# Performance work log

Hardware: AMD Instinct MI355X
Metric: run time of the kernel (lower is better)

The kernel has to match this reference:

```python
import jax, jax.numpy as jnp
import numpy as np

WINDOW_SIZES = [4, 8, 12]
BN_EPS = 1e-5


def conv1x1(x, w, b):
    # x: [B,C,H,W], w: [O,C], b: [O]
    return jnp.einsum('bchw,oc->bohw', x, w) + b[None, :, None, None]


def bnorm(x, gamma, beta, mean, var):
    inv = gamma * jax.lax.rsqrt(var + BN_EPS)
    return (x - mean[None, :, None, None]) * inv[None, :, None, None] + beta[None, :, None, None]


def shift5(x):
    # ShiftConv2d1 depthwise fixed-weight conv == 4-direction zero-padded shift + identity
    b, c, H, W = x.shape
    g = c // 5
    p = jnp.pad(x, ((0, 0), (0, 0), (1, 1), (1, 1)))
    return jnp.concatenate([
        p[:, 0 * g:1 * g, 1:-1, 2:],    # kernel[1,2]: x[i, j+1]
        p[:, 1 * g:2 * g, 1:-1, :-2],   # kernel[1,0]: x[i, j-1]
        p[:, 2 * g:3 * g, 2:, 1:-1],    # kernel[2,1]: x[i+1, j]
        p[:, 3 * g:4 * g, :-2, 1:-1],   # kernel[0,1]: x[i-1, j]
        p[:, 4 * g:, 1:-1, 1:-1],       # kernel[1,1]: identity
    ], axis=1)


def lfe(x, w0, b0, w1, b1):
    y = jax.nn.relu(conv1x1(shift5(x), w0, b0))
    return conv1x1(shift5(y), w1, b1)


def win_part(x, ws):
    # [B,C,H,W] -> [B*nh*nw, ws*ws, C]
    b, c, H, W = x.shape
    x = x.reshape(b, c, H // ws, ws, W // ws, ws)
    return x.transpose(0, 2, 4, 3, 5, 1).reshape(b * (H // ws) * (W // ws), ws * ws, c)


def win_merge(y, ws, b, H, W):
    # [B*nh*nw, ws*ws, C] -> [B,C,H,W]
    c = y.shape[-1]
    y = y.reshape(b, H // ws, W // ws, ws, ws, c)
    return y.transpose(0, 5, 1, 3, 2, 4).reshape(b, c, H, W)


def gmsa_first(x, pi_w, pi_b, bn_g, bn_b, bn_m, bn_v, po_w, po_b):
    b, c, H, W = x.shape
    xp = bnorm(conv1x1(x, pi_w, pi_b), bn_g, bn_b, bn_m, bn_v)
    ch = 2 * c // 3
    ys, atns = [], []
    for i, ws in enumerate(WINDOW_SIZES):
        x_ = xp[:, i * ch:(i + 1) * ch]
        x_ = jnp.roll(x_, (-(ws // 2), -(ws // 2)), axis=(2, 3))
        qv = win_part(x_, ws)                      # [nw, ws*ws, 2*cc]
        cc = ch // 2
        q, v = qv[..., :cc], qv[..., cc:]
        atn = jax.nn.softmax(q @ q.transpose(0, 2, 1), axis=-1)
        y_ = win_merge(atn @ v, ws, b, H, W)
        y_ = jnp.roll(y_, (ws // 2, ws // 2), axis=(2, 3))
        ys.append(y_)
        atns.append(atn)
    return conv1x1(jnp.concatenate(ys, axis=1), po_w, po_b), atns


def gmsa_shared(x, atns, pi_w, pi_b, bn_g, bn_b, bn_m, bn_v, po_w, po_b):
    b, c, H, W = x.shape
    xp = bnorm(conv1x1(x, pi_w, pi_b), bn_g, bn_b, bn_m, bn_v)
    ch = c // 3
    ys = []
    for i, ws in enumerate(WINDOW_SIZES):
        x_ = jnp.roll(xp[:, i * ch:(i + 1) * ch], (-(ws // 2), -(ws // 2)), axis=(2, 3))
        v = win_part(x_, ws)
        y_ = win_merge(atns[i] @ v, ws, b, H, W)
        ys.append(jnp.roll(y_, (ws // 2, ws // 2), axis=(2, 3)))
    return conv1x1(jnp.concatenate(ys, axis=1), po_w, po_b)


def setup_inputs() -> dict:
    key = jax.random.key(0)
    ks = jax.random.split(key, 20)
    B, C, H, W = 4, 60, 384, 384
    E = 2 * C  # exp_ratio=2 hidden width
    s = 0.05

    def rn(k, shape):
        return jax.random.normal(k, shape, dtype=jnp.float32) * s

    return {
        'x': jax.random.normal(ks[0], (B, C, H, W), dtype=jnp.float32),
        # LFE 0
        'lfe0_w0': rn(ks[1], (E, C)), 'lfe0_b0': jnp.zeros((E,), jnp.float32),
        'lfe0_w1': rn(ks[2], (C, E)), 'lfe0_b1': jnp.zeros((C,), jnp.float32),
        # GMSA 0 (calc_attn=True): project_inp C->2C, BN(2C), project_out C->C
        'g0_pi_w': rn(ks[3], (2 * C, C)), 'g0_pi_b': jnp.zeros((2 * C,), jnp.float32),
        'g0_bn_g': jnp.ones((2 * C,), jnp.float32), 'g0_bn_b': jnp.zeros((2 * C,), jnp.float32),
        'g0_bn_m': jnp.zeros((2 * C,), jnp.float32), 'g0_bn_v': jnp.ones((2 * C,), jnp.float32),
        'g0_po_w': rn(ks[4], (C, C)), 'g0_po_b': jnp.zeros((C,), jnp.float32),
        # LFE 1
        'lfe1_w0': rn(ks[5], (E, C)), 'lfe1_b0': jnp.zeros((E,), jnp.float32),
        'lfe1_w1': rn(ks[6], (C, E)), 'lfe1_b1': jnp.zeros((C,), jnp.float32),
        # GMSA 1 (calc_attn=False): project_inp C->C, BN(C), project_out C->C
        'g1_pi_w': rn(ks[7], (C, C)), 'g1_pi_b': jnp.zeros((C,), jnp.float32),
        'g1_bn_g': jnp.ones((C,), jnp.float32), 'g1_bn_b': jnp.zeros((C,), jnp.float32),
        'g1_bn_m': jnp.zeros((C,), jnp.float32), 'g1_bn_v': jnp.ones((C,), jnp.float32),
        'g1_po_w': rn(ks[8], (C, C)), 'g1_po_b': jnp.zeros((C,), jnp.float32),
    }


def reference(x, lfe0_w0, lfe0_b0, lfe0_w1, lfe0_b1,
              g0_pi_w, g0_pi_b, g0_bn_g, g0_bn_b, g0_bn_m, g0_bn_v, g0_po_w, g0_po_b,
              lfe1_w0, lfe1_b0, lfe1_w1, lfe1_b1,
              g1_pi_w, g1_pi_b, g1_bn_g, g1_bn_b, g1_bn_m, g1_bn_v, g1_po_w, g1_po_b):
    # depth 0
    x = lfe(x, lfe0_w0, lfe0_b0, lfe0_w1, lfe0_b1) + x
    y, atns = gmsa_first(x, g0_pi_w, g0_pi_b, g0_bn_g, g0_bn_b, g0_bn_m, g0_bn_v, g0_po_w, g0_po_b)
    x = y + x
    # shared depth 1 (reuses attention maps)
    x = lfe(x, lfe1_w0, lfe1_b0, lfe1_w1, lfe1_b1) + x
    y = gmsa_shared(x, atns, g1_pi_w, g1_pi_b, g1_bn_g, g1_bn_b, g1_bn_m, g1_bn_v, g1_po_w, g1_po_b)
    return y + x
```

## Files before the change

### kernel.cpp

```cpp
#include <hip/hip_runtime.h>
#include <math.h>

constexpr int B_ = 4, C_ = 60, H_ = 384, W_ = 384;
constexpr int HW_ = H_ * W_;
constexpr int NC_ = B_ * C_ * HW_;
constexpr int NE_ = B_ * 120 * HW_;

typedef __attribute__((ext_vector_type(8))) short short8;
typedef __attribute__((ext_vector_type(4))) float f32x4;
typedef __attribute__((ext_vector_type(4))) unsigned short u16x4;

__device__ __forceinline__ unsigned short f2b(float f) {
    unsigned u = __builtin_bit_cast(unsigned, f);
    unsigned r = (u + 0x7fff + ((u >> 16) & 1)) >> 16;
    return (unsigned short)r;
}
__device__ __forceinline__ float b2f(unsigned short s) {
    return __builtin_bit_cast(float, (unsigned)s << 16);
}

__device__ __forceinline__ int xcd_swz(int bid, int nwg) {
    const int q = nwg >> 3, r = nwg & 7;
    const int xcd = bid & 7, off = bid >> 3;
    return (xcd < r ? xcd * (q + 1) : r * (q + 1) + (xcd - r) * q) + off;
}

struct PrepJobs {
    const float* src[8];
    unsigned short* dst[8];
    int cin[8];
    int cout[8];
};

__global__ __launch_bounds__(256) void prep_all(PrepJobs J)
{
    int bid = blockIdx.x;
    #pragma unroll 1
    for (int j = 0; j < 8; ++j) {
        const int KP = J.cin[j]  > 64 ? 128 : 64;
        const int MP = J.cout[j] > 64 ? 128 : 64;
        const int nb = MP * KP / 256;
        if (bid < nb) {
            const int i = bid * 256 + threadIdx.x;
            const int o = i / KP, c = i - o * KP;
            const float v = (o < J.cout[j] && c < J.cin[j]) ? J.src[j][o * J.cin[j] + c] : 0.f;
            J.dst[j][o * KP + (c ^ ((o & 7) << 3))] = f2b(v);
            return;
        }
        bid -= nb;
    }
}

struct ABJobs {
    const float* bias[8];
    const float* g[8];
    const float* bb[8];
    const float* m[8];
    const float* v[8];
    float* dst[8];
    int cout[8];
};

__global__ __launch_bounds__(256) void prep_ab(ABJobs J)
{
    const int j = blockIdx.x;
    const int n = J.cout[j];
    for (int o = threadIdx.x; o < n; o += 256) {
        float A = 1.f, Bv = J.bias[j][o];
        if (J.g[j]) {
            const float s = J.g[j][o] * rsqrtf(J.v[j][o] + 1e-5f);
            A  = s;
            Bv = (Bv - J.m[j][o]) * s + J.bb[j][o];
        }
        J.dst[j][o]     = A;
        J.dst[j][n + o] = Bv;
    }
}

template<int KP>
__device__ __forceinline__ int lds_off(int px, int cb) {
    return px * (KP * 2) + (cb ^ ((px & 7) << 4) ^ (((px >> 3) & 1) << 6));
}

template<int CIN, int COUT, int GSH, bool SRCB, bool RELU, bool RESID,
         bool RESIDB, bool OUTB>
__global__ __launch_bounds__(512, 6)
void conv_g(const void* __restrict__ in_, const unsigned short* __restrict__ wp,
            const float* __restrict__ AB,
            const void* __restrict__ resid_, void* __restrict__ out_)
{
    constexpr int KP  = CIN  > 64 ? 128 : 64;
    constexpr int MP  = COUT > 64 ? 128 : 64;
    constexpr int NNT = MP / 16;
    constexpr int KBL = KP / 32;
    __shared__ __align__(16) char xlds[128 * KP * 2];

    const int tid = threadIdx.x;
    const int n0  = blockIdx.x * 128;
    const int b   = n0 / HW_;
    const int p0  = n0 - b * HW_;
    const int hh  = p0 / W_;
    const int ww0 = p0 - hh * W_;

    for (int task = tid; task < (KP / 2) * 16; task += 512) {
        const int oct = (task >> 4) & 15;
        const int pr  = (task & 15) | ((task >> 8) << 4);
        const int c0  = pr * 2;
        const int s0  = oct * 8;

        if (c0 >= CIN) {
            #pragma unroll
            for (int i = 0; i < 8; ++i)
                *(unsigned*)(xlds + lds_off<KP>(s0 + i, c0 * 2)) = 0u;
            continue;
        }

        int dh = 0, dw = 0;
        if (GSH > 0) {
            const int grp = c0 / GSH;
            dh = (grp == 2) ? 1 : ((grp == 3) ? -1 : 0);
            dw = (grp == 0) ? 1 : ((grp == 1) ? -1 : 0);
        }
        const int h2 = hh + dh;
        const bool vh = (unsigned)h2 < (unsigned)H_;
        const long eoff = (long)(b * CIN + c0) * HW_ + h2 * W_ + ww0 + s0;

        unsigned short va[8], vb[8];
        if (vh) {
            if constexpr (SRCB) {
                const unsigned short* p = (const unsigned short*)in_;
                short8 A = *(const short8*)(p + eoff);
                short8 Bv = *(const short8*)(p + eoff + HW_);
                #pragma unroll
                for (int i = 0; i < 8; ++i) { va[i] = (unsigned short)A[i]; vb[i] = (unsigned short)Bv[i]; }
            } else {
                const float* p = (const float*)in_;
                f32x4 A0 = *(const f32x4*)(p + eoff);
                f32x4 A1 = *(const f32x4*)(p + eoff + 4);
                f32x4 B0 = *(const f32x4*)(p + eoff + HW_);
                f32x4 B1 = *(const f32x4*)(p + eoff + HW_ + 4);
                #pragma unroll
                for (int i = 0; i < 4; ++i) {
                    va[i] = f2b(A0[i]); va[i + 4] = f2b(A1[i]);
                    vb[i] = f2b(B0[i]); vb[i + 4] = f2b(B1[i]);
                }
            }
        } else {
            #pragma unroll
            for (int i = 0; i < 8; ++i) { va[i] = 0; vb[i] = 0; }
        }
        #pragma unroll
        for (int i = 0; i < 8; ++i) {
            const int px = s0 + i - dw;
            if ((unsigned)px < 128u) {
                const unsigned v = (unsigned)va[i] | ((unsigned)vb[i] << 16);
                *(unsigned*)(xlds + lds_off<KP>(px, c0 * 2)) = v;
            }
        }
        if (GSH > 0 && dw != 0) {
            const bool hndl = (dw == 1) ? (oct == 15) : (oct == 0);
            if (hndl) {
                const int px_e = (dw == 1) ? 127 : 0;
                const int w_abs = ww0 + px_e + dw;
                unsigned short ua = 0, ub = 0;
                if (vh && (unsigned)w_abs < (unsigned)W_) {
                    const long e2 = (long)(b * CIN + c0) * HW_ + h2 * W_ + w_abs;
                    if constexpr (SRCB) {
                        ua = ((const unsigned short*)in_)[e2];
                        ub = ((const unsigned short*)in_)[e2 + HW_];
                    } else {
                        ua = f2b(((const float*)in_)[e2]);
                        ub = f2b(((const float*)in_)[e2 + HW_]);
                    }
                }
                *(unsigned*)(xlds + lds_off<KP>(px_e, c0 * 2)) =
                    (unsigned)ua | ((unsigned)ub << 16);
            }
        }
    }
    __syncthreads();

    const int wv = tid >> 6, lo = tid & 15, hi = (tid & 63) >> 4;
    f32x4 acc[NNT];
    #pragma unroll
    for (int nt = 0; nt < NNT; ++nt) acc[nt] = f32x4{0.f, 0.f, 0.f, 0.f};

    #pragma unroll
    for (int kb = 0; kb < KBL; ++kb) {
        const int row = wv * 16 + lo;
        const short8 a = *(const short8*)(xlds + lds_off<KP>(row, kb * 64 + hi * 16));
        #pragma unroll
        for (int nt = 0; nt < NNT; ++nt) {
            const int wrow = nt * 16 + lo;
            const short8 bb = *(const short8*)((const char*)wp +
                      wrow * (KP * 2) + ((kb * 64 + hi * 16) ^ ((wrow & 7) << 4)));
            acc[nt] = __builtin_amdgcn_mfma_f32_16x16x32_bf16(a, bb, acc[nt], 0, 0, 0);
        }
    }

    const int px0 = p0 + wv * 16 + hi * 4;
    #pragma unroll
    for (int nt = 0; nt < NNT; ++nt) {
        const int ch = nt * 16 + lo;
        if (ch < COUT) {
            const long oi = (long)(b * COUT + ch) * HW_ + px0;
            float v[4];
            f32x4 rf;
            u16x4 rb;
            if (RESID) {
                if (RESIDB) rb = *(const u16x4*)((const unsigned short*)resid_ + oi);
                else        rf = *(const f32x4*)((const float*)resid_ + oi);
            }
            #pragma unroll
            for (int r = 0; r < 4; ++r) {
                float t = fmaf(acc[nt][r], AB[ch], AB[COUT + ch]);
                if (RELU) t = fmaxf(t, 0.f);
                if (RESID) t += RESIDB ? b2f(rb[r]) : rf[r];
                v[r] = t;
            }
            if (OUTB) {
                u16x4 o4;
                #pragma unroll
                for (int r = 0; r < 4; ++r) o4[r] = f2b(v[r]);
                *(u16x4*)((unsigned short*)out_ + oi) = o4;
            } else {
                *(f32x4*)((float*)out_ + oi) = f32x4{v[0], v[1], v[2], v[3]};
            }
        }
    }
}

template<int WS, int WPB>
__global__ __launch_bounds__(256)
void attn_m(const unsigned short* __restrict__ qsrc, int qC, int qbase,
            const unsigned short* __restrict__ vsrc, int vC, int vbase,
            unsigned short* __restrict__ out, int obase)
{
    constexpr int P     = WS * WS;
    constexpr int NMT   = P / 16;
    constexpr int S     = WS / 2;
    constexpr int WGX   = W_ / WS;
    constexpr int WGY   = H_ / WS;
    constexpr int NWIN  = WGY * WGX;
    constexpr int QP    = 40;
    constexpr int KP2   = ((P + 31) / 32) * 32;
    constexpr int VP    = KP2 + 8;
    constexpr int KB2   = KP2 / 32;
    constexpr int TILES = WPB * NMT;

    __shared__ __align__(16) unsigned short Qs[WPB * P * QP];
    __shared__ __align__(16) unsigned short VTs[WPB * 32 * VP];
    __shared__ __align__(16) unsigned short Ps[WPB * P * VP];
    __shared__ float rs[WPB * P];

    const int tid = threadIdx.x;
    const int blk = xcd_swz(blockIdx.x, gridDim.x);

    for (int i = tid; i < WPB * P * 6; i += 256) {
        const int row = i / 6, j = i - (i / 6) * 6;
        *(unsigned*)&Qs[row * QP + 20 + 2 * j] = 0u;
    }
    for (int i = tid; i < WPB * 12 * (KP2 / 2); i += 256) {
        const int rr = i / (KP2 / 2), j = i - rr * (KP2 / 2);
        const int win = rr / 12, ch = 20 + (rr - (rr / 12) * 12);
        *(unsigned*)&VTs[(win * 32 + ch) * VP + 2 * j] = 0u;
    }
    if constexpr (KP2 > P) {
        for (int i = tid; i < WPB * 20 * ((KP2 - P) / 2); i += 256) {
            const int rr = i / ((KP2 - P) / 2), j = i - rr * ((KP2 - P) / 2);
            const int win = rr / 20, ch = rr - (rr / 20) * 20;
            *(unsigned*)&VTs[(win * 32 + ch) * VP + P + 2 * j] = 0u;
        }
        for (int i = tid; i < WPB * P * ((KP2 - P) / 2); i += 256) {
            const int row = i / ((KP2 - P) / 2), j = i - row * ((KP2 - P) / 2);
            *(unsigned*)&Ps[row * VP + P + 2 * j] = 0u;
        }
    }
    for (int e = tid; e < WPB * P * 20; e += 256) {
        const int win = e / (P * 20);
        const int rem = e - win * (P * 20);
        const int ch  = rem / P;
        const int pos = rem - ch * P;
        const int gw  = blk * WPB + win;
        const int b   = gw / NWIN;
        const int rwin = gw - b * NWIN;
        const int wh = rwin / WGX, ww = rwin - (rwin / WGX) * WGX;
        const int pr = pos / WS,  pc = pos - (pos / WS) * WS;
        int hs = wh * WS + pr + S; if (hs >= H_) hs -= H_;
        int wd = ww * WS + pc + S; if (wd >= W_) wd -= W_;
        const long off = (long)hs * W_ + wd;
        Qs [(win * P  + pos) * QP + ch ] = qsrc[(long)(b * qC + qbase + ch) * HW_ + off];
        VTs[(win * 32 + ch ) * VP + pos] = vsrc[(long)(b * vC + vbase + ch) * HW_ + off];
    }
    __syncthreads();

    const int wv = tid >> 6, lo = tid & 15, hi = (tid & 63) >> 4;

    for (int t = wv; t < TILES; t += 4) {
        const int win = t / NMT, mt = t - (t / NMT) * NMT;
        const unsigned short* Qw = Qs + win * P * QP;
        unsigned short* Pw = Ps + win * P * VP;

        const short8 af = *(const short8*)(Qw + (mt * 16 + lo) * QP + hi * 8);
        f32x4 a1[NMT];
        #pragma unroll
        for (int nt = 0; nt < NMT; ++nt) a1[nt] = f32x4{0.f, 0.f, 0.f, 0.f};
        #pragma unroll
        for (int nt = 0; nt < NMT; ++nt) {
            const short8 bf = *(const short8*)(Qw + (nt * 16 + lo) * QP + hi * 8);
            a1[nt] = __builtin_amdgcn_mfma_f32_16x16x32_bf16(af, bf, a1[nt], 0, 0, 0);
        }
        float psum[4] = {0.f, 0.f, 0.f, 0.f};
        #pragma unroll
        for (int nt = 0; nt < NMT; ++nt) {
            #pragma unroll
            for (int r = 0; r < 4; ++r) {
                const float p = __expf(a1[nt][r]);
                psum[r] += p;
                Pw[(mt * 16 + hi * 4 + r) * VP + nt * 16 + lo] = f2b(p);
            }
        }
        #pragma unroll
        for (int r = 0; r < 4; ++r) {
            psum[r] += __shfl_xor(psum[r], 1);
            psum[r] += __shfl_xor(psum[r], 2);
            psum[r] += __shfl_xor(psum[r], 4);
            psum[r] += __shfl_xor(psum[r], 8);
        }
        if (lo == 0) {
            #pragma unroll
            for (int r = 0; r < 4; ++r)
                rs[win * P + mt * 16 + hi * 4 + r] = psum[r];
        }
    }
    __syncthreads();

    for (int t = wv; t < TILES; t += 4) {
        const int win = t / NMT, qt = t - (t / NMT) * NMT;
        const unsigned short* Vw = VTs + win * 32 * VP;
        const unsigned short* Pw = Ps + win * P * VP;

        f32x4 a2[2];
        a2[0] = f32x4{0.f, 0.f, 0.f, 0.f};
        a2[1] = f32x4{0.f, 0.f, 0.f, 0.f};
        #pragma unroll
        for (int kb = 0; kb < KB2; ++kb) {
            const short8 bf = *(const short8*)(Pw + (qt * 16 + lo) * VP + kb * 32 + hi * 8);
            #pragma unroll
            for (int m2 = 0; m2 < 2; ++m2) {
                const short8 af = *(const short8*)(Vw + (m2 * 16 + lo) * VP + kb * 32 + hi * 8);
                a2[m2] = __builtin_amdgcn_mfma_f32_16x16x32_bf16(af, bf, a2[m2], 0, 0, 0);
            }
        }
        const int gw = blk * WPB + win;
        const int b  = gw / NWIN;
        const int rwin = gw - b * NWIN;
        const int wh = rwin / WGX, ww = rwin - (rwin / WGX) * WGX;

        const int row = qt * 16 + lo;
        const float inv = 1.f / rs[win * P + row];
        const int pr = row / WS, pc = row - (row / WS) * WS;
        int hs = wh * WS + pr + S; if (hs >= H_) hs -= H_;
        int wd = ww * WS + pc + S; if (wd >= W_) wd -= W_;
        const long pbase = (long)(b * 60 + obase) * HW_ + (long)hs * W_ + wd;
        #pragma unroll
        for (int m2 = 0; m2 < 2; ++m2) {
            #pragma unroll
            for (int r = 0; r < 4; ++r) {
                const int ch = m2 * 16 + hi * 4 + r;
                if (ch < 20)
                    out[pbase + (long)ch * HW_] = f2b(a2[m2][r] * inv);
            }
        }
    }
}

extern "C" void kernel_launch(void* const* d_in, const int* in_sizes, int n_in,
                              void* d_out, int out_size, void* d_ws, size_t ws_size,
                              hipStream_t stream)
{
    const float* x     = (const float*)d_in[0];
    const float* l0w0  = (const float*)d_in[1];
    const float* l0b0  = (const float*)d_in[2];
    const float* l0w1  = (const float*)d_in[3];
    const float* l0b1  = (const float*)d_in[4];
    const float* g0piw = (const float*)d_in[5];
    const float* g0pib = (const float*)d_in[6];
    const float* g0bng = (const float*)d_in[7];
    const float* g0bnb = (const float*)d_in[8];
    const float* g0bnm = (const float*)d_in[9];
    const float* g0bnv = (const float*)d_in[10];
    const float* g0pow = (const float*)d_in[11];
    const float* g0pob = (const float*)d_in[12];
    const float* l1w0  = (const float*)d_in[13];
    const float* l1b0  = (const float*)d_in[14];
    const float* l1w1  = (const float*)d_in[15];
    const float* l1b1  = (const float*)d_in[16];
    const float* g1piw = (const float*)d_in[17];
    const float* g1pib = (const float*)d_in[18];
    const float* g1bng = (const float*)d_in[19];
    const float* g1bnb = (const float*)d_in[20];
    const float* g1bnm = (const float*)d_in[21];
    const float* g1bnv = (const float*)d_in[22];
    const float* g1pow = (const float*)d_in[23];
    const float* g1pob = (const float*)d_in[24];

    unsigned short* HID = (unsigned short*)d_ws;
    unsigned short* XPB = HID + NE_;
    unsigned short* XP1 = XPB + NE_;
    unsigned short* YS1 = XP1 + NC_;
    unsigned short* CCB = YS1 + NC_;
    unsigned short* WP  = CCB + NC_;
    float*          ABF = (float*)(WP + 53248);
    float* OUTF  = (float*)d_out;
    unsigned short* YS0 = (unsigned short*)d_out;

    unsigned short* W1  = WP;
    unsigned short* W2  = WP + 8192;
    unsigned short* W3  = WP + 16384;
    unsigned short* W5  = WP + 24576;
    unsigned short* W6  = WP + 28672;
    unsigned short* W7  = WP + 36864;
    unsigned short* W8  = WP + 45056;
    unsigned short* W10 = WP + 49152;

    float* AB1  = ABF;
    float* AB2  = ABF + 240;
    float* AB3  = ABF + 360;
    float* AB5  = ABF + 600;
    float* AB6  = ABF + 720;
    float* AB7  = ABF + 960;
    float* AB8  = ABF + 1080;
    float* AB10 = ABF + 1200;

    PrepJobs J;
    J.src[0]=l0w0;  J.dst[0]=W1;  J.cin[0]=60;  J.cout[0]=120;
    J.src[1]=l0w1;  J.dst[1]=W2;  J.cin[1]=120; J.cout[1]=60;
    J.src[2]=g0piw; J.dst[2]=W3;  J.cin[2]=60;  J.cout[2]=120;
    J.src[3]=g0pow; J.dst[3]=W5;  J.cin[3]=60;  J.cout[3]=60;
    J.src[4]=l1w0;  J.dst[4]=W6;  J.cin[4]=60;  J.cout[4]=120;
    J.src[5]=l1w1;  J.dst[5]=W7;  J.cin[5]=120; J.cout[5]=60;
    J.src[6]=g1piw; J.dst[6]=W8;  J.cin[6]=60;  J.cout[6]=60;
    J.src[7]=g1pow; J.dst[7]=W10; J.cin[7]=60;  J.cout[7]=60;
    prep_all<<<208, 256, 0, stream>>>(J);

    ABJobs A;
    for (int j = 0; j < 8; ++j) { A.g[j]=nullptr; A.bb[j]=nullptr; A.m[j]=nullptr; A.v[j]=nullptr; }
    A.bias[0]=l0b0;  A.dst[0]=AB1;  A.cout[0]=120;
    A.bias[1]=l0b1;  A.dst[1]=AB2;  A.cout[1]=60;
    A.bias[2]=g0pib; A.dst[2]=AB3;  A.cout[2]=120; A.g[2]=g0bng; A.bb[2]=g0bnb; A.m[2]=g0bnm; A.v[2]=g0bnv;
    A.bias[3]=g0pob; A.dst[3]=AB5;  A.cout[3]=60;
    A.bias[4]=l1b0;  A.dst[4]=AB6;  A.cout[4]=120;
    A.bias[5]=l1b1;  A.dst[5]=AB7;  A.cout[5]=60;
    A.bias[6]=g1pib; A.dst[6]=AB8;  A.cout[6]=60;  A.g[6]=g1bng; A.bb[6]=g1bnb; A.m[6]=g1bnm; A.v[6]=g1bnv;
    A.bias[7]=g1pob; A.dst[7]=AB10; A.cout[7]=60;
    prep_ab<<<8, 256, 0, stream>>>(A);

    dim3 cblk(512);
    dim3 gconv(B_ * HW_ / 128);
    dim3 blk(256);

    conv_g<60,120,12,false,true,false,false,true><<<gconv,cblk,0,stream>>>(
        x, W1, AB1, nullptr, HID);
    conv_g<120,60,24,true,false,true,false,true><<<gconv,cblk,0,stream>>>(
        HID, W2, AB2, x, CCB);
    conv_g<60,120,0,true,false,false,false,true><<<gconv,cblk,0,stream>>>(
        CCB, W3, AB3, nullptr, XPB);
    attn_m<4,4><<<dim3(9216),blk,0,stream>>>(XPB,120,0,   XPB,120,20,  YS0, 0);
    attn_m<8,1><<<dim3(9216),blk,0,stream>>>(XPB,120,40,  XPB,120,60,  YS0,20);
    attn_m<12,1><<<dim3(4096),blk,0,stream>>>(XPB,120,80, XPB,120,100, YS0,40);
    conv_g<60,60,0,true,false,true,true,true><<<gconv,cblk,0,stream>>>(
        YS0, W5, AB5, CCB, CCB);
    conv_g<60,120,12,true,true,false,false,true><<<gconv,cblk,0,stream>>>(
        CCB, W6, AB6, nullptr, HID);
    conv_g<120,60,24,true,false,true,true,true><<<gconv,cblk,0,stream>>>(
        HID, W7, AB7, CCB, CCB);
    conv_g<60,60,0,true,false,false,false,true><<<gconv,cblk,0,stream>>>(
        CCB, W8, AB8, nullptr, XP1);
    attn_m<4,4><<<dim3(9216),blk,0,stream>>>(XPB,120,0,  XP1,60,0,  YS1, 0);
    attn_m<8,1><<<dim3(9216),blk,0,stream>>>(XPB,120,40, XP1,60,20, YS1,20);
    attn_m<12,1><<<dim3(4096),blk,0,stream>>>(XPB,120,80,XP1,60,40, YS1,40);
    conv_g<60,60,0,true,false,true,true,false><<<gconv,cblk,0,stream>>>(
        YS1, W10, AB10, CCB, OUTF);
}
```

Measured before the change: 995.4 us.

## Make conv blocks persistent over several tiles with register double-buffered prefetch

Each 1x1 conv block now processes T=3 consecutive 128-pixel tiles. The next tile's global loads go into registers while the current tile runs its MFMA and epilogue. Residual loads are hoisted ahead of the MFMA loop so their latency overlaps compute. This hides global load latency behind compute and cuts the block count. In exchange it uses more registers (the launch-bounds occupancy hint drops from 6 to 4), launches a third as many blocks, and adds an extra barrier per tile.

```diff
diff --git a/kernel.cpp b/kernel.cpp
--- a/kernel.cpp
+++ b/kernel.cpp
@@ -82,39 +82,28 @@
     return px * (KP * 2) + (cb ^ ((px & 7) << 4) ^ (((px >> 3) & 1) << 6));
 }
 
-template<int CIN, int COUT, int GSH, bool SRCB, bool RELU, bool RESID,
-         bool RESIDB, bool OUTB>
-__global__ __launch_bounds__(512, 6)
-void conv_g(const void* __restrict__ in_, const unsigned short* __restrict__ wp,
-            const float* __restrict__ AB,
-            const void* __restrict__ resid_, void* __restrict__ out_)
-{
-    constexpr int KP  = CIN  > 64 ? 128 : 64;
-    constexpr int MP  = COUT > 64 ? 128 : 64;
-    constexpr int NNT = MP / 16;
-    constexpr int KBL = KP / 32;
-    __shared__ __align__(16) char xlds[128 * KP * 2];
-
-    const int tid = threadIdx.x;
-    const int n0  = blockIdx.x * 128;
+template<int CIN, int GSH, bool SRCB, int KP, int NTASK>
+__device__ __forceinline__ void stage_load(const void* __restrict__ in_, int tile,
+        int tid, unsigned (&w)[NTASK][8], unsigned (&edge)[NTASK])
+{
+    const int n0  = tile * 128;
     const int b   = n0 / HW_;
     const int p0  = n0 - b * HW_;
     const int hh  = p0 / W_;
     const int ww0 = p0 - hh * W_;
-
-    for (int task = tid; task < (KP / 2) * 16; task += 512) {
+    #pragma unroll
+    for (int i = 0; i < NTASK; ++i) {
+        const int task = tid + 512 * i;
         const int oct = (task >> 4) & 15;
         const int pr  = (task & 15) | ((task >> 8) << 4);
         const int c0  = pr * 2;
-        const int s0  = oct * 8;
-
+        edge[i] = 0;
         if (c0 >= CIN) {
             #pragma unroll
-            for (int i = 0; i < 8; ++i)
-                *(unsigned*)(xlds + lds_off<KP>(s0 + i, c0 * 2)) = 0u;
+            for (int j = 0; j < 8; ++j) w[i][j] = 0u;
             continue;
         }
-
+        const int s0 = oct * 8;
         int dh = 0, dw = 0;
         if (GSH > 0) {
             const int grp = c0 / GSH;
@@ -123,16 +112,17 @@
         }
         const int h2 = hh + dh;
         const bool vh = (unsigned)h2 < (unsigned)H_;
-        const long eoff = (long)(b * CIN + c0) * HW_ + h2 * W_ + ww0 + s0;
-
-        unsigned short va[8], vb[8];
+        const long eoff = (long)(b * CIN + c0) * HW_ + (long)h2 * W_ + ww0 + s0;
+
         if (vh) {
             if constexpr (SRCB) {
                 const unsigned short* p = (const unsigned short*)in_;
                 short8 A = *(const short8*)(p + eoff);
                 short8 Bv = *(const short8*)(p + eoff + HW_);
                 #pragma unroll
-                for (int i = 0; i < 8; ++i) { va[i] = (unsigned short)A[i]; vb[i] = (unsigned short)Bv[i]; }
+                for (int j = 0; j < 8; ++j)
+                    w[i][j] = (unsigned)(unsigned short)A[j] |
+                              ((unsigned)(unsigned short)Bv[j] << 16);
             } else {
                 const float* p = (const float*)in_;
                 f32x4 A0 = *(const f32x4*)(p + eoff);
@@ -140,22 +130,14 @@
                 f32x4 B0 = *(const f32x4*)(p + eoff + HW_);
                 f32x4 B1 = *(const f32x4*)(p + eoff + HW_ + 4);
                 #pragma unroll
-                for (int i = 0; i < 4; ++i) {
-                    va[i] = f2b(A0[i]); va[i + 4] = f2b(A1[i]);
-                    vb[i] = f2b(B0[i]); vb[i + 4] = f2b(B1[i]);
+                for (int j = 0; j < 4; ++j) {
+                    w[i][j]     = (unsigned)f2b(A0[j]) | ((unsigned)f2b(B0[j]) << 16);
+                    w[i][j + 4] = (unsigned)f2b(A1[j]) | ((unsigned)f2b(B1[j]) << 16);
                 }
             }
         } else {
             #pragma unroll
-            for (int i = 0; i < 8; ++i) { va[i] = 0; vb[i] = 0; }
-        }
-        #pragma unroll
-        for (int i = 0; i < 8; ++i) {
-            const int px = s0 + i - dw;
-            if ((unsigned)px < 128u) {
-                const unsigned v = (unsigned)va[i] | ((unsigned)vb[i] << 16);
-                *(unsigned*)(xlds + lds_off<KP>(px, c0 * 2)) = v;
-            }
+            for (int j = 0; j < 8; ++j) w[i][j] = 0u;
         }
         if (GSH > 0 && dw != 0) {
             const bool hndl = (dw == 1) ? (oct == 15) : (oct == 0);
@@ -164,7 +146,7 @@
                 const int w_abs = ww0 + px_e + dw;
                 unsigned short ua = 0, ub = 0;
                 if (vh && (unsigned)w_abs < (unsigned)W_) {
-                    const long e2 = (long)(b * CIN + c0) * HW_ + h2 * W_ + w_abs;
+                    const long e2 = (long)(b * CIN + c0) * HW_ + (long)h2 * W_ + w_abs;
                     if constexpr (SRCB) {
                         ua = ((const unsigned short*)in_)[e2];
                         ub = ((const unsigned short*)in_)[e2 + HW_];
@@ -173,60 +155,137 @@
                         ub = f2b(((const float*)in_)[e2 + HW_]);
                     }
                 }
-                *(unsigned*)(xlds + lds_off<KP>(px_e, c0 * 2)) =
-                    (unsigned)ua | ((unsigned)ub << 16);
-            }
-        }
-    }
-    __syncthreads();
-
+                edge[i] = (unsigned)ua | ((unsigned)ub << 16);
+            }
+        }
+    }
+}
+
+template<int CIN, int GSH, int KP, int NTASK>
+__device__ __forceinline__ void stage_write(int tid,
+        const unsigned (&w)[NTASK][8], const unsigned (&edge)[NTASK], char* xlds)
+{
+    #pragma unroll
+    for (int i = 0; i < NTASK; ++i) {
+        const int task = tid + 512 * i;
+        const int oct = (task >> 4) & 15;
+        const int pr  = (task & 15) | ((task >> 8) << 4);
+        const int c0  = pr * 2;
+        const int s0  = oct * 8;
+        int dw = 0;
+        if (GSH > 0 && c0 < CIN) {
+            const int grp = c0 / GSH;
+            dw = (grp == 0) ? 1 : ((grp == 1) ? -1 : 0);
+        }
+        #pragma unroll
+        for (int j = 0; j < 8; ++j) {
+            const int px = s0 + j - dw;
+            if ((unsigned)px < 128u)
+                *(unsigned*)(xlds + lds_off<KP>(px, c0 * 2)) = w[i][j];
+        }
+        if (GSH > 0 && dw != 0) {
+            const bool hndl = (dw == 1) ? (oct == 15) : (oct == 0);
+            if (hndl) {
+                const int px_e = (dw == 1) ? 127 : 0;
+                *(unsigned*)(xlds + lds_off<KP>(px_e, c0 * 2)) = edge[i];
+            }
+        }
+    }
+}
+
+template<int CIN, int COUT, int GSH, bool SRCB, bool RELU, bool RESID,
+         bool RESIDB, bool OUTB, int T>
+__global__ __launch_bounds__(512, 4)
+void conv_g(const void* __restrict__ in_, const unsigned short* __restrict__ wp,
+            const float* __restrict__ AB,
+            const void* __restrict__ resid_, void* __restrict__ out_)
+{
+    constexpr int KP    = CIN  > 64 ? 128 : 64;
+    constexpr int MP    = COUT > 64 ? 128 : 64;
+    constexpr int NNT   = MP / 16;
+    constexpr int KBL   = KP / 32;
+    constexpr int NTASK = (KP / 2) * 16 / 512;
+    __shared__ __align__(16) char xlds[128 * KP * 2];
+
+    const int tid = threadIdx.x;
+    const int nt0 = blockIdx.x * T;
     const int wv = tid >> 6, lo = tid & 15, hi = (tid & 63) >> 4;
-    f32x4 acc[NNT];
+
+    unsigned wA[NTASK][8], eA[NTASK];
+    unsigned wB[NTASK][8], eB[NTASK];
+    stage_load<CIN, GSH, SRCB, KP, NTASK>(in_, nt0, tid, wA, eA);
+
     #pragma unroll
-    for (int nt = 0; nt < NNT; ++nt) acc[nt] = f32x4{0.f, 0.f, 0.f, 0.f};
-
-    #pragma unroll
-    for (int kb = 0; kb < KBL; ++kb) {
-        const int row = wv * 16 + lo;
-        const short8 a = *(const short8*)(xlds + lds_off<KP>(row, kb * 64 + hi * 16));
+    for (int t = 0; t < T; ++t) {
+        const int tile = nt0 + t;
+        const int n0 = tile * 128;
+        const int b  = n0 / HW_;
+        const int p0 = n0 - b * HW_;
+
+        if (t & 1) stage_write<CIN, GSH, KP, NTASK>(tid, wB, eB, xlds);
+        else       stage_write<CIN, GSH, KP, NTASK>(tid, wA, eA, xlds);
+        __syncthreads();
+        if (t + 1 < T) {
+            if (t & 1) stage_load<CIN, GSH, SRCB, KP, NTASK>(in_, tile + 1, tid, wA, eA);
+            else       stage_load<CIN, GSH, SRCB, KP, NTASK>(in_, tile + 1, tid, wB, eB);
+        }
+
+        const int px0 = p0 + wv * 16 + hi * 4;
+
+        u16x4 rb[NNT]; f32x4 rf[NNT];
+        if (RESID) {
+            #pragma unroll
+            for (int nt = 0; nt < NNT; ++nt) {
+                const int ch = nt * 16 + lo;
+                if (ch < COUT) {
+                    const long oi = (long)(b * COUT + ch) * HW_ + px0;
+                    if (RESIDB) rb[nt] = *(const u16x4*)((const unsigned short*)resid_ + oi);
+                    else        rf[nt] = *(const f32x4*)((const float*)resid_ + oi);
+                }
+            }
+        }
+
+        f32x4 acc[NNT];
+        #pragma unroll
+        for (int nt = 0; nt < NNT; ++nt) acc[nt] = f32x4{0.f, 0.f, 0.f, 0.f};
+
+        #pragma unroll
+        for (int kb = 0; kb < KBL; ++kb) {
+            const int row = wv * 16 + lo;
+            const short8 a = *(const short8*)(xlds + lds_off<KP>(row, kb * 64 + hi * 16));
+            #pragma unroll
+            for (int nt = 0; nt < NNT; ++nt) {
+                const int wrow = nt * 16 + lo;
+                const short8 bb = *(const short8*)((const char*)wp +
+                          wrow * (KP * 2) + ((kb * 64 + hi * 16) ^ ((wrow & 7) << 4)));
+                acc[nt] = __builtin_amdgcn_mfma_f32_16x16x32_bf16(a, bb, acc[nt], 0, 0, 0);
+            }
+        }
+
         #pragma unroll
         for (int nt = 0; nt < NNT; ++nt) {
-            const int wrow = nt * 16 + lo;
-            const short8 bb = *(const short8*)((const char*)wp +
-                      wrow * (KP * 2) + ((kb * 64 + hi * 16) ^ ((wrow & 7) << 4)));
-            acc[nt] = __builtin_amdgcn_mfma_f32_16x16x32_bf16(a, bb, acc[nt], 0, 0, 0);
-        }
-    }
-
-    const int px0 = p0 + wv * 16 + hi * 4;
-    #pragma unroll
-    for (int nt = 0; nt < NNT; ++nt) {
-        const int ch = nt * 16 + lo;
-        if (ch < COUT) {
-            const long oi = (long)(b * COUT + ch) * HW_ + px0;
-            float v[4];
-            f32x4 rf;
-            u16x4 rb;
-            if (RESID) {
-                if (RESIDB) rb = *(const u16x4*)((const unsigned short*)resid_ + oi);
-                else        rf = *(const f32x4*)((const float*)resid_ + oi);
-            }
-            #pragma unroll
-            for (int r = 0; r < 4; ++r) {
-                float t = fmaf(acc[nt][r], AB[ch], AB[COUT + ch]);
-                if (RELU) t = fmaxf(t, 0.f);
-                if (RESID) t += RESIDB ? b2f(rb[r]) : rf[r];
-                v[r] = t;
-            }
-            if (OUTB) {
-                u16x4 o4;
+            const int ch = nt * 16 + lo;
+            if (ch < COUT) {
+                const long oi = (long)(b * COUT + ch) * HW_ + px0;
+                float v[4];
                 #pragma unroll
-                for (int r = 0; r < 4; ++r) o4[r] = f2b(v[r]);
-                *(u16x4*)((unsigned short*)out_ + oi) = o4;
-            } else {
-                *(f32x4*)((float*)out_ + oi) = f32x4{v[0], v[1], v[2], v[3]};
-            }
-        }
+                for (int r = 0; r < 4; ++r) {
+                    float tt = fmaf(acc[nt][r], AB[ch], AB[COUT + ch]);
+                    if (RELU) tt = fmaxf(tt, 0.f);
+                    if (RESID) tt += RESIDB ? b2f(rb[nt][r]) : rf[nt][r];
+                    v[r] = tt;
+                }
+                if (OUTB) {
+                    u16x4 o4;
+                    #pragma unroll
+                    for (int r = 0; r < 4; ++r) o4[r] = f2b(v[r]);
+                    *(u16x4*)((unsigned short*)out_ + oi) = o4;
+                } else {
+                    *(f32x4*)((float*)out_ + oi) = f32x4{v[0], v[1], v[2], v[3]};
+                }
+            }
+        }
+        if (t + 1 < T) __syncthreads();
     }
 }
 
@@ -456,30 +515,31 @@
     A.bias[7]=g1pob; A.dst[7]=AB10; A.cout[7]=60;
     prep_ab<<<8, 256, 0, stream>>>(A);
 
+    constexpr int T = 3;
     dim3 cblk(512);
-    dim3 gconv(B_ * HW_ / 128);
+    dim3 gconv(B_ * HW_ / 128 / T);
     dim3 blk(256);
 
-    conv_g<60,120,12,false,true,false,false,true><<<gconv,cblk,0,stream>>>(
+    conv_g<60,120,12,false,true,false,false,true,T><<<gconv,cblk,0,stream>>>(
         x, W1, AB1, nullptr, HID);
-    conv_g<120,60,24,true,false,true,false,true><<<gconv,cblk,0,stream>>>(
+    conv_g<120,60,24,true,false,true,false,true,T><<<gconv,cblk,0,stream>>>(
         HID, W2, AB2, x, CCB);
-    conv_g<60,120,0,true,false,false,false,true><<<gconv,cblk,0,stream>>>(
+    conv_g<60,120,0,true,false,false,false,true,T><<<gconv,cblk,0,stream>>>(
         CCB, W3, AB3, nullptr, XPB);
     attn_m<4,4><<<dim3(9216),blk,0,stream>>>(XPB,120,0,   XPB,120,20,  YS0, 0);
     attn_m<8,1><<<dim3(9216),blk,0,stream>>>(XPB,120,40,  XPB,120,60,  YS0,20);
     attn_m<12,1><<<dim3(4096),blk,0,stream>>>(XPB,120,80, XPB,120,100, YS0,40);
-    conv_g<60,60,0,true,false,true,true,true><<<gconv,cblk,0,stream>>>(
+    conv_g<60,60,0,true,false,true,true,true,T><<<gconv,cblk,0,stream>>>(
         YS0, W5, AB5, CCB, CCB);
-    conv_g<60,120,12,true,true,false,false,true><<<gconv,cblk,0,stream>>>(
+    conv_g<60,120,12,true,true,false,false,true,T><<<gconv,cblk,0,stream>>>(
         CCB, W6, AB6, nullptr, HID);
-    conv_g<120,60,24,true,false,true,true,true><<<gconv,cblk,0,stream>>>(
+    conv_g<120,60,24,true,false,true,true,true,T><<<gconv,cblk,0,stream>>>(
         HID, W7, AB7, CCB, CCB);
-    conv_g<60,60,0,true,false,false,false,true><<<gconv,cblk,0,stream>>>(
+    conv_g<60,60,0,true,false,false,false,true,T><<<gconv,cblk,0,stream>>>(
         CCB, W8, AB8, nullptr, XP1);
     attn_m<4,4><<<dim3(9216),blk,0,stream>>>(XPB,120,0,  XP1,60,0,  YS1, 0);
     attn_m<8,1><<<dim3(9216),blk,0,stream>>>(XPB,120,40, XP1,60,20, YS1,20);
     attn_m<12,1><<<dim3(4096),blk,0,stream>>>(XPB,120,80,XP1,60,40, YS1,40);
-    conv_g<60,60,0,true,false,true,true,false><<<gconv,cblk,0,stream>>>(
+    conv_g<60,60,0,true,false,true,true,false,T><<<gconv,cblk,0,stream>>>(
         YS1, W10, AB10, CCB, OUTF);
 }
```

After: 1.133 ms. +13.9%, slower.
